# Performance work log

Hardware: AMD Instinct MI355X
Metric: run time of the kernel (lower is better)

## Reference

```python
import jax, jax.numpy as jnp
import numpy as np

L, H, C = 2, 8, 128          # layers, heads, hidden_channels
D = C // H                   # head dim
NPAT, NICD, NNDC = 50000, 591, 2042
OUT = 90
E = 250000                   # edges per relation
# edge relations as (src_type, dst_type); node types: 0=patient, 1=icd, 2=ndc
ETYPES = [(0, 1), (1, 0), (0, 2), (2, 0)]


def _seg_softmax(logits, seg, n):
    # softmax over edges grouped by destination node (PyG `softmax`)
    m = jax.ops.segment_max(logits, seg, num_segments=n)
    e = jnp.exp(logits - m[seg])
    s = jax.ops.segment_sum(e, seg, num_segments=n)
    return e / s[seg]


def setup_inputs() -> dict:
    key = jax.random.key(0)
    ks = jax.random.split(key, 24)
    s = 1.0 / np.sqrt(C)
    n = lambda k, shape, sc: jax.random.normal(k, shape, dtype=jnp.float32) * sc
    return {
        "x_patient": n(ks[0], (NPAT, C), 1.0),
        "w_in_patient": n(ks[1], (C, C), s),
        "b_in_patient": jnp.zeros((C,), jnp.float32),
        "emb_icd": n(ks[2], (NICD, C), 0.1),
        "emb_ndc": n(ks[3], (NNDC, C), 0.1),
        "kw": n(ks[4], (L, 3, C, C), s), "kb": jnp.zeros((L, 3, C), jnp.float32),
        "qw": n(ks[5], (L, 3, C, C), s), "qb": jnp.zeros((L, 3, C), jnp.float32),
        "vw": n(ks[6], (L, 3, C, C), s), "vb": jnp.zeros((L, 3, C), jnp.float32),
        "aw": n(ks[7], (L, 3, C, C), s), "ab": jnp.zeros((L, 3, C), jnp.float32),
        "skip": jnp.ones((L, 3), jnp.float32),
        "a_rel": n(ks[8], (L, 4, H, D, D), 1.0 / np.sqrt(D)),
        "m_rel": n(ks[9], (L, 4, H, D, D), 1.0 / np.sqrt(D)),
        "p_rel": jnp.ones((L, 4, H), jnp.float32),
        "w_out": n(ks[10], (C, OUT), s),
        "b_out": jnp.zeros((OUT,), jnp.float32),
        "x_icd": jnp.arange(NICD, dtype=jnp.int32),
        "x_ndc": jnp.arange(NNDC, dtype=jnp.int32),
        "src_pi": jax.random.randint(ks[11], (E,), 0, NPAT, dtype=jnp.int32),
        "dst_pi": jax.random.randint(ks[12], (E,), 0, NICD, dtype=jnp.int32),
        "src_ip": jax.random.randint(ks[13], (E,), 0, NICD, dtype=jnp.int32),
        "dst_ip": jax.random.randint(ks[14], (E,), 0, NPAT, dtype=jnp.int32),
        "src_pn": jax.random.randint(ks[15], (E,), 0, NPAT, dtype=jnp.int32),
        "dst_pn": jax.random.randint(ks[16], (E,), 0, NNDC, dtype=jnp.int32),
        "src_np": jax.random.randint(ks[17], (E,), 0, NNDC, dtype=jnp.int32),
        "dst_np": jax.random.randint(ks[18], (E,), 0, NPAT, dtype=jnp.int32),
    }


def reference(x_patient, w_in_patient, b_in_patient, emb_icd, emb_ndc,
              kw, kb, qw, qb, vw, vb, aw, ab, skip,
              a_rel, m_rel, p_rel, w_out, b_out,
              x_icd, x_ndc,
              src_pi, dst_pi, src_ip, dst_ip, src_pn, dst_pn, src_np, dst_np):
    edges = [(src_pi, dst_pi), (src_ip, dst_ip), (src_pn, dst_pn), (src_np, dst_np)]
    sizes = [NPAT, NICD, NNDC]
    # per-type input projection / embedding + relu
    x = [jax.nn.relu(x_patient @ w_in_patient + b_in_patient),
         jax.nn.relu(emb_icd[x_icd]),
         jax.nn.relu(emb_ndc[x_ndc])]
    scale = 1.0 / np.sqrt(D)
    for l in range(L):
        k = [(x[t] @ kw[l, t] + kb[l, t]).reshape(-1, H, D) for t in range(3)]
        q = [(x[t] @ qw[l, t] + qb[l, t]).reshape(-1, H, D) for t in range(3)]
        v = [(x[t] @ vw[l, t] + vb[l, t]).reshape(-1, H, D) for t in range(3)]
        agg = [jnp.zeros((sizes[t], H, D), x[0].dtype) for t in range(3)]
        for r, (st, dt) in enumerate(ETYPES):
            src, dst = edges[r]
            kr = jnp.einsum('nhd,hde->nhe', k[st], a_rel[l, r])  # relation key transform
            vr = jnp.einsum('nhd,hde->nhe', v[st], m_rel[l, r])  # relation msg transform
            alpha = jnp.sum(q[dt][dst] * kr[src], axis=-1) * p_rel[l, r] * scale  # [E,H]
            alpha = _seg_softmax(alpha, dst, sizes[dt])
            agg[dt] = agg[dt] + jax.ops.segment_sum(vr[src] * alpha[:, :, None], dst, num_segments=sizes[dt])
        new_x = []
        for t in range(3):
            o = jax.nn.gelu(agg[t].reshape(-1, C)) @ aw[l, t] + ab[l, t]
            a = jax.nn.sigmoid(skip[l, t])
            new_x.append(a * o + (1.0 - a) * x[t])  # learned skip (dims match)
        x = new_x
    return jax.nn.sigmoid(x[0] @ w_out + b_out)
```

## Files before the change

kernel.cpp:

```cpp
#include <hip/hip_runtime.h>
#include <math.h>

#define CDIM  128
#define NHEAD 8
#define DHEAD 16
#define NPAT  50000
#define NICD  591
#define NNDC  2042
#define OUTN  90
#define NEDGE 250000
#define NLAYER 2
#define ALC   640

#define OFF0  0
#define OFF1  (NICD)
#define OFF2  (NICD + NPAT)
#define OFF3  (NICD + NPAT + NNDC)
#define NTOT  (NICD + NPAT + NNDC + NPAT)
#define NB_SCAN ((NTOT + 1023) / 1024)

#define LDP 40
#define CTILE 72
#define LOG2E 1.4426950408889634f

#define NSEG  (2 * NNDC)
#define NAGG  ((NPAT + 3) / 4)

#define PB_W  224
#define PB_C  (PB_W + 16)
#define PB_Q  (PB_C + 3)
#define PB_Z  (PB_Q + NB_SCAN)
#define PB_G  (PB_Z + (((NICD + NNDC) * CDIM + 255) / 256))

#define SCAT_PER 64
#define SCAT_N   (4 * SCAT_PER)
#define INP_NWG  (((NPAT + 63) / 64) * 2)

typedef __attribute__((ext_vector_type(8))) short bf16x8;
typedef __attribute__((ext_vector_type(4))) float f32x4;

__device__ __forceinline__ float gelu_fast(float x) {
    float x3 = x * x * x;
    float y = 0.7978845608028654f * (x + 0.044715f * x3);
    float e = exp2f(y * (2.0f * LOG2E));
    float t = 1.0f - 2.0f * __builtin_amdgcn_rcpf(e + 1.0f);
    return 0.5f * x * (1.0f + t);
}
__device__ __forceinline__ float b2f(unsigned short u) {
    union { unsigned int i; float f; } v; v.i = ((unsigned int)u) << 16; return v.f;
}
__device__ __forceinline__ unsigned short f2b(float f) {
    union { float ff; unsigned int i; } v; v.ff = f;
    unsigned int i = v.i;
    return (unsigned short)((i + 0x7FFFu + ((i >> 16) & 1u)) >> 16);
}
__device__ __forceinline__ float2 b2x2(unsigned int u) {
    union { unsigned int i; float f; } lo, hi;
    lo.i = u << 16; hi.i = u & 0xFFFF0000u;
    return make_float2(lo.f, hi.f);
}

__device__ __forceinline__ void gemm_core(
    const unsigned short* __restrict__ Ap,
    const unsigned short* __restrict__ Wt, const float* __restrict__ bias,
    unsigned short* __restrict__ Cp, int ldc,
    int M, int N, int ntile, int wgid,
    const unsigned short* __restrict__ xold,
    const float* __restrict__ skipv, int skipidx,
    unsigned short* Al, unsigned short* Bl, unsigned short* Cst)
{
    int bm = (wgid / ntile) * 64, bn = (wgid % ntile) * 64;
    int t = threadIdx.x;
    int lane = t & 63, w = t >> 6;
    int wr = w >> 1, wc = w & 1;
    int quad = lane >> 4, lm = lane & 15;
    f32x4 acc[2][2] = {};
    const int srow = t >> 2;
    const int skq  = (t & 3) * 8;

    for (int k0 = 0; k0 < 128; k0 += 32) {
        {
            int row = bm + srow;
            uint4 u = make_uint4(0, 0, 0, 0);
            if (row < M)
                u = *(const uint4*)(Ap + (size_t)row * 128 + k0 + skq);
            *(uint4*)&Al[srow * LDP + skq] = u;
        }
        {
            int n = bn + srow;
            uint4 u = make_uint4(0, 0, 0, 0);
            if (n < N) u = *(const uint4*)(Wt + (size_t)n * 128 + k0 + skq);
            *(uint4*)&Bl[srow * LDP + skq] = u;
        }
        __syncthreads();
        bf16x8 af[2], bfr[2];
        #pragma unroll
        for (int i = 0; i < 2; i++) {
            af[i]  = *(const bf16x8*)&Al[(wr * 32 + i * 16 + lm) * LDP + quad * 8];
            bfr[i] = *(const bf16x8*)&Bl[(wc * 32 + i * 16 + lm) * LDP + quad * 8];
        }
        acc[0][0] = __builtin_amdgcn_mfma_f32_16x16x32_bf16(af[0], bfr[0], acc[0][0], 0, 0, 0);
        acc[0][1] = __builtin_amdgcn_mfma_f32_16x16x32_bf16(af[0], bfr[1], acc[0][1], 0, 0, 0);
        acc[1][0] = __builtin_amdgcn_mfma_f32_16x16x32_bf16(af[1], bfr[0], acc[1][0], 0, 0, 0);
        acc[1][1] = __builtin_amdgcn_mfma_f32_16x16x32_bf16(af[1], bfr[1], acc[1][1], 0, 0, 0);
        __syncthreads();
    }

    float aSk = 0.f, oneM = 0.f;
    if (skipv) {
        float sv = skipv[skipidx];
        aSk = 1.0f / (1.0f + expf(-sv));
        oneM = 1.0f - aSk;
    }
    #pragma unroll
    for (int tm = 0; tm < 2; tm++)
    #pragma unroll
    for (int tn = 0; tn < 2; tn++)
    #pragma unroll
    for (int r = 0; r < 4; r++) {
        int lrow = wr * 32 + tm * 16 + quad * 4 + r;
        int lcol = wc * 32 + tn * 16 + lm;
        int row = bm + lrow, col = bn + lcol;
        float v = acc[tm][tn][r] + (bias ? bias[col] : 0.f);
        if (skipv && row < M) v = aSk * v + oneM * b2f(xold[(size_t)row * ldc + col]);
        Cst[lrow * CTILE + lcol] = f2b(v);
    }
    __syncthreads();
    int row = t >> 2, seg = (t & 3) * 16;
    if (bm + row < M) {
        unsigned short* dst = Cp + (size_t)(bm + row) * ldc + bn + seg;
        *(uint4*)dst       = *(const uint4*)&Cst[row * CTILE + seg];
        *(uint4*)(dst + 8) = *(const uint4*)&Cst[row * CTILE + seg + 8];
    }
}

__device__ __forceinline__ void gemm3_body(
    int g,
    const unsigned short* A0, const unsigned short* W0,
    const float* b0, unsigned short* C0, int M0, int N0, int ntile0, int nwg0,
    const unsigned short* A1, const unsigned short* W1,
    const float* b1, unsigned short* C1, int M1, int N1, int ntile1, int nwg01,
    const unsigned short* A2, const unsigned short* W2,
    const float* b2, unsigned short* C2, int M2, int N2, int ntile2,
    const float* skipv, int si0, int si1, int si2,
    unsigned short* Al, unsigned short* Bl, unsigned short* Cst)
{
    if (g < nwg0) {
        int qq = nwg0 >> 3, rr = nwg0 & 7;
        int xcd = g & 7, idx = g >> 3;
        int wgid = (xcd < rr ? xcd * (qq + 1) : rr * (qq + 1) + (xcd - rr) * qq) + idx;
        gemm_core(A0, W0, b0, C0, N0, M0, N0, ntile0, wgid, C0, skipv, si0, Al, Bl, Cst);
    } else if (g < nwg01) {
        gemm_core(A1, W1, b1, C1, N1, M1, N1, ntile1, g - nwg0, C1, skipv, si1, Al, Bl, Cst);
    } else {
        gemm_core(A2, W2, b2, C2, N2, M2, N2, ntile2, g - nwg01, C2, skipv, si2, Al, Bl, Cst);
    }
}

__global__ __launch_bounds__(256) void gemm3_kernel(
    const unsigned short* __restrict__ A0, const unsigned short* __restrict__ W0,
    const float* __restrict__ b0, unsigned short* __restrict__ C0,
    int M0, int N0, int ntile0, int nwg0,
    const unsigned short* __restrict__ A1, const unsigned short* __restrict__ W1,
    const float* __restrict__ b1, unsigned short* __restrict__ C1,
    int M1, int N1, int ntile1, int nwg01,
    const unsigned short* __restrict__ A2, const unsigned short* __restrict__ W2,
    const float* __restrict__ b2, unsigned short* __restrict__ C2,
    int M2, int N2, int ntile2,
    const float* __restrict__ skipv, int si0, int si1, int si2)
{
    __shared__ unsigned short Al[64 * LDP];
    __shared__ unsigned short Bl[64 * LDP];
    __shared__ unsigned short Cst[64 * CTILE];
    gemm3_body(blockIdx.x, A0, W0, b0, C0, M0, N0, ntile0, nwg0,
               A1, W1, b1, C1, M1, N1, ntile1, nwg01,
               A2, W2, b2, C2, M2, N2, ntile2,
               skipv, si0, si1, si2, Al, Bl, Cst);
}

__device__ __forceinline__ void input_proj_body(
    int u, char* smem,
    const float* __restrict__ Axp, const unsigned short* __restrict__ Wtin,
    const float* __restrict__ b_in, unsigned short* __restrict__ xb0)
{
    unsigned short* Al = (unsigned short*)smem;
    unsigned short* Bl = Al + 64 * LDP;
    unsigned short* Cst = Bl + 64 * LDP;
    int t = threadIdx.x;
    int nwg = INP_NWG;
    int qq = nwg >> 3, rr = nwg & 7;
    int xcd = u & 7, idx = u >> 3;
    int wgid = (xcd < rr ? xcd * (qq + 1) : rr * (qq + 1) + (xcd - rr) * qq) + idx;
    int bm = (wgid >> 1) * 64, bn = (wgid & 1) * 64;

    int lane = t & 63, w = t >> 6;
    int wr = w >> 1, wc = w & 1;
    int quad = lane >> 4, lm = lane & 15;
    f32x4 acc[2][2] = {};
    const int srow = t >> 2;
    const int skq  = (t & 3) * 8;

    for (int k0 = 0; k0 < 128; k0 += 32) {
        {
            int row = bm + srow;
            float f[8] = {0.f,0.f,0.f,0.f,0.f,0.f,0.f,0.f};
            if (row < NPAT) {
                const float4* ap = (const float4*)(Axp + (size_t)row * 128 + k0 + skq);
                float4 u0 = ap[0], u1 = ap[1];
                f[0]=u0.x; f[1]=u0.y; f[2]=u0.z; f[3]=u0.w;
                f[4]=u1.x; f[5]=u1.y; f[6]=u1.z; f[7]=u1.w;
            }
            unsigned short v[8];
            for (int i = 0; i < 8; i++) v[i] = f2b(f[i]);
            *(uint4*)&Al[srow * LDP + skq] = *(uint4*)v;
        }
        {
            int n = bn + srow;
            *(uint4*)&Bl[srow * LDP + skq] = *(const uint4*)(Wtin + (size_t)n * 128 + k0 + skq);
        }
        __syncthreads();
        bf16x8 af[2], bfr[2];
        #pragma unroll
        for (int i = 0; i < 2; i++) {
            af[i]  = *(const bf16x8*)&Al[(wr * 32 + i * 16 + lm) * LDP + quad * 8];
            bfr[i] = *(const bf16x8*)&Bl[(wc * 32 + i * 16 + lm) * LDP + quad * 8];
        }
        acc[0][0] = __builtin_amdgcn_mfma_f32_16x16x32_bf16(af[0], bfr[0], acc[0][0], 0, 0, 0);
        acc[0][1] = __builtin_amdgcn_mfma_f32_16x16x32_bf16(af[0], bfr[1], acc[0][1], 0, 0, 0);
        acc[1][0] = __builtin_amdgcn_mfma_f32_16x16x32_bf16(af[1], bfr[0], acc[1][0], 0, 0, 0);
        acc[1][1] = __builtin_amdgcn_mfma_f32_16x16x32_bf16(af[1], bfr[1], acc[1][1], 0, 0, 0);
        __syncthreads();
    }
    #pragma unroll
    for (int tm = 0; tm < 2; tm++)
    #pragma unroll
    for (int tn = 0; tn < 2; tn++)
    #pragma unroll
    for (int r = 0; r < 4; r++) {
        int lrow = wr * 32 + tm * 16 + quad * 4 + r;
        int lcol = wc * 32 + tn * 16 + lm;
        float v = acc[tm][tn][r] + b_in[bn + lcol];
        v = fmaxf(v, 0.f);
        Cst[lrow * CTILE + lcol] = f2b(v);
    }
    __syncthreads();
    int row = t >> 2, seg = (t & 3) * 16;
    if (bm + row < NPAT) {
        unsigned short* dst = xb0 + (size_t)(bm + row) * 128 + bn + seg;
        *(uint4*)dst       = *(const uint4*)&Cst[row * CTILE + seg];
        *(uint4*)(dst + 8) = *(const uint4*)&Cst[row * CTILE + seg + 8];
    }
}

__device__ __forceinline__ void scatter_body(
    int b, char* smem,
    const int* s0, const int* d0, const int* s1, const int* d1,
    const int* s2, const int* d2, const int* s3, const int* d3,
    int* cursor, unsigned int* es)
{
    int t = threadIdx.x;
    int* lcnt = (int*)smem;
    int* lbase = lcnt + 2048;
    int rel = b / SCAT_PER;
    int bx = b % SCAT_PER;
    const int* sp = (rel == 0) ? s0 : (rel == 1) ? s1 : (rel == 2) ? s2 : s3;
    const int* dp = (rel == 0) ? d0 : (rel == 1) ? d1 : (rel == 2) ? d2 : d3;
    int off = (rel == 0) ? OFF0 : (rel == 1) ? OFF1 : (rel == 2) ? OFF2 : OFF3;
    if (rel == 1 || rel == 3) {
        for (int e = bx * 256 + t; e < NEDGE; e += SCAT_PER * 256) {
            int d = dp[e];
            int p = atomicAdd(&cursor[off + d], 1);
            es[p] = ((unsigned int)sp[e] << 16) | (unsigned int)d;
        }
    } else {
        int nb = (rel == 0) ? NICD : NNDC;
        int per = (NEDGE + SCAT_PER - 1) / SCAT_PER;
        int e0 = bx * per, e1 = min(e0 + per, NEDGE);
        for (int i = t; i < nb; i += 256) lcnt[i] = 0;
        __syncthreads();
        for (int e = e0 + t; e < e1; e += 256) atomicAdd(&lcnt[dp[e]], 1);
        __syncthreads();
        for (int i = t; i < nb; i += 256) {
            int c = lcnt[i];
            lbase[i] = c ? atomicAdd(&cursor[off + i], c) : 0;
            lcnt[i] = 0;
        }
        __syncthreads();
        for (int e = e0 + t; e < e1; e += 256) {
            int d = dp[e];
            int p = lbase[d] + atomicAdd(&lcnt[d], 1);
            es[p] = ((unsigned int)sp[e] << 16) | (unsigned int)d;
        }
    }
}

__global__ __launch_bounds__(256) void hist_in_kernel(
    const int* __restrict__ d0, const int* __restrict__ d1,
    const int* __restrict__ d2, const int* __restrict__ d3,
    int* __restrict__ deg,
    const float* __restrict__ Axp, const unsigned short* __restrict__ Wtin,
    const float* __restrict__ b_in, unsigned short* __restrict__ xb0)
{
    __shared__ __align__(16) char smem[19456];
    int b = blockIdx.x;
    int t = threadIdx.x;
    if (b < 256) {
        int* lh = (int*)smem;
        int rel = b >> 6;
        int bx = b & 63;
        const int* dp = (rel == 0) ? d0 : (rel == 1) ? d1 : (rel == 2) ? d2 : d3;
        int off = (rel == 0) ? OFF0 : (rel == 1) ? OFF1 : (rel == 2) ? OFF2 : OFF3;
        if (rel == 1 || rel == 3) {
            for (int e = bx * 256 + t; e < NEDGE; e += 64 * 256)
                atomicAdd(&deg[off + dp[e]], 1);
        } else {
            int nb = (rel == 0) ? NICD : NNDC;
            for (int i = t; i < nb; i += 256) lh[i] = 0;
            __syncthreads();
            for (int e = bx * 256 + t; e < NEDGE; e += 64 * 256)
                atomicAdd(&lh[dp[e]], 1);
            __syncthreads();
            for (int i = t; i < nb; i += 256) {
                int v = lh[i];
                if (v) atomicAdd(&deg[off + i], v);
            }
        }
    } else {
        input_proj_body(b - 256, smem, Axp, Wtin, b_in, xb0);
// ... 47 lines not shown
    int qq = nwg >> 3, rr = nwg & 7;
    int xcd = orig & 7, idx = orig >> 3;
    int wgid = (xcd < rr ? xcd * (qq + 1) : rr * (qq + 1) + (xcd - rr) * qq) + idx;
    int bm = (wgid / ntile) * 64, bn = (wgid % ntile) * 64;

    int t = threadIdx.x;
    int lane = t & 63, w = t >> 6;
    int wr = w >> 1, wc = w & 1;
    int quad = lane >> 4, lm = lane & 15;
    f32x4 acc[2][2] = {};
    const int srow = t >> 2;
    const int skq  = (t & 3) * 8;

    for (int k0 = 0; k0 < 128; k0 += 32) {
        {
            int row = bm + srow;
            uint4 u = make_uint4(0, 0, 0, 0);
            if (a_mode == 0) {
                if (row < M)
                    u = *(const uint4*)((const unsigned short*)Ap + (size_t)row * lda + k0 + skq);
            } else {
                float f[8] = {0.f,0.f,0.f,0.f,0.f,0.f,0.f,0.f};
                if (row < M) {
                    const float4* ap = (const float4*)((const float*)Ap + (size_t)row * lda + k0 + skq);
                    float4 u0 = ap[0], u1 = ap[1];
                    f[0]=u0.x; f[1]=u0.y; f[2]=u0.z; f[3]=u0.w;
                    f[4]=u1.x; f[5]=u1.y; f[6]=u1.z; f[7]=u1.w;
                }
                unsigned short v[8];
                for (int i = 0; i < 8; i++) v[i] = f2b(f[i]);
                u = *(uint4*)v;
            }
            *(uint4*)&Al[srow * LDP + skq] = u;
        }
        {
            int n = bn + srow;
            uint4 u = make_uint4(0, 0, 0, 0);
            if (n < N) u = *(const uint4*)(Wt + (size_t)n * 128 + k0 + skq);
            *(uint4*)&Bl[srow * LDP + skq] = u;
        }
        __syncthreads();
        bf16x8 af[2], bfr[2];
        #pragma unroll
        for (int i = 0; i < 2; i++) {
            af[i]  = *(const bf16x8*)&Al[(wr * 32 + i * 16 + lm) * LDP + quad * 8];
            bfr[i] = *(const bf16x8*)&Bl[(wc * 32 + i * 16 + lm) * LDP + quad * 8];
        }
        acc[0][0] = __builtin_amdgcn_mfma_f32_16x16x32_bf16(af[0], bfr[0], acc[0][0], 0, 0, 0);
        acc[0][1] = __builtin_amdgcn_mfma_f32_16x16x32_bf16(af[0], bfr[1], acc[0][1], 0, 0, 0);
        acc[1][0] = __builtin_amdgcn_mfma_f32_16x16x32_bf16(af[1], bfr[0], acc[1][0], 0, 0, 0);
        acc[1][1] = __builtin_amdgcn_mfma_f32_16x16x32_bf16(af[1], bfr[1], acc[1][1], 0, 0, 0);
        __syncthreads();
    }

    if (c_mode == 0) {
        #pragma unroll
        for (int tm = 0; tm < 2; tm++)
        #pragma unroll
        for (int tn = 0; tn < 2; tn++)
        #pragma unroll
        for (int r = 0; r < 4; r++) {
            int lrow = wr * 32 + tm * 16 + quad * 4 + r;
            int lcol = wc * 32 + tn * 16 + lm;
            int col = bn + lcol;
            float v = acc[tm][tn][r] + (bias ? bias[col] : 0.f);
            if (act == 1) v = fmaxf(v, 0.f);
            Cst[lrow * CTILE + lcol] = f2b(v);
        }
        __syncthreads();
        int row = t >> 2, seg = (t & 3) * 16;
        if (bm + row < M) {
            unsigned short* dst = (unsigned short*)Cp + (size_t)(bm + row) * ldc + bn + seg;
            *(uint4*)dst       = *(const uint4*)&Cst[row * CTILE + seg];
            *(uint4*)(dst + 8) = *(const uint4*)&Cst[row * CTILE + seg + 8];
        }
    } else {
        #pragma unroll
        for (int tm = 0; tm < 2; tm++)
        #pragma unroll
        for (int tn = 0; tn < 2; tn++)
        #pragma unroll
        for (int r = 0; r < 4; r++) {
            int row = bm + wr * 32 + tm * 16 + quad * 4 + r;
            int col = bn + wc * 32 + tn * 16 + lm;
            if (row >= M || col >= N) continue;
            float v = acc[tm][tn][r] + (bias ? bias[col] : 0.f);
            if (act == 1) v = fmaxf(v, 0.f);
            else if (act == 2) v = 1.0f / (1.0f + expf(-v));
            ((float*)Cp)[(size_t)row * ldc + col] = v;
        }
    }
}

__global__ __launch_bounds__(256) void prep_all_kernel(
    const float* __restrict__ qw, const float* __restrict__ aw,
    const float* __restrict__ w_in, const float* __restrict__ w_out,
    unsigned short* __restrict__ Wb0, unsigned short* __restrict__ Wb1,
    unsigned short* __restrict__ Wb2, unsigned short* __restrict__ Wtaw,
    unsigned short* __restrict__ Wtin, unsigned short* __restrict__ Wtout,
    const float* __restrict__ kw, const float* __restrict__ vw,
    const float* __restrict__ a_rel, const float* __restrict__ m_rel,
    const float* __restrict__ kb, const float* __restrict__ vb,
    float* __restrict__ bb0, float* __restrict__ bb1, float* __restrict__ bb2,
    const float* __restrict__ qb,
    int* __restrict__ deg,
    const float* __restrict__ emb_icd, const int* __restrict__ x_icd,
    unsigned short* __restrict__ xb1,
    const float* __restrict__ emb_ndc, const int* __restrict__ x_ndc,
    unsigned short* __restrict__ xb2)
{
    __shared__ float tile[32][33];
    int b = blockIdx.x;
    int tid = threadIdx.x;
    if (b < PB_W) {
        int z = b >> 4, rem = b & 15;
        int by = rem >> 2, bx = rem & 3;
        const float* s; unsigned short* d; int N = 128;
        if (z < 2)       { s = qw + (size_t)z * 3 * 16384;               d = Wb0 + (size_t)z * 640 * 128; }
        else if (z < 4)  { s = qw + 16384 + (size_t)(z - 2) * 3 * 16384; d = Wb1 + (size_t)(z - 2) * 384 * 128; }
        else if (z < 6)  { s = qw + 2 * 16384 + (size_t)(z - 4) * 3 * 16384; d = Wb2 + (size_t)(z - 4) * 384 * 128; }
        else if (z < 12) { s = aw + (size_t)(z - 6) * 16384;             d = Wtaw + (size_t)(z - 6) * 16384; }
        else if (z == 12){ s = w_in;  d = Wtin; }
        else             { s = w_out; d = Wtout; N = OUTN; }
        int k0 = bx * 32, n0 = by * 32;
        int tx = tid & 31, ty = tid >> 5;
        for (int i = 0; i < 32; i += 8) {
            int k = k0 + ty + i, n = n0 + tx;
            tile[ty + i][tx] = (k < 128 && n < N) ? s[(size_t)k * N + n] : 0.f;
        }
        __syncthreads();
        for (int i = 0; i < 32; i += 8) {
            int n = n0 + ty + i, k = k0 + tx;
            if (n < N && k < 128) d[(size_t)n * 128 + k] = f2b(tile[tx][ty + i]);
        }
    } else if (b < PB_C) {
        int s = b - PB_W;
        int l = s >> 3, j = s & 7;
        int ty, isV, r, rowoff, nw;
        unsigned short* Wb; float* bb;
        switch (j) {
          case 0: ty=0; isV=0; r=0; Wb=Wb0; bb=bb0; rowoff=128; nw=640; break;
          case 1: ty=0; isV=1; r=0; Wb=Wb0; bb=bb0; rowoff=256; nw=640; break;
          case 2: ty=0; isV=0; r=2; Wb=Wb0; bb=bb0; rowoff=384; nw=640; break;
          case 3: ty=0; isV=1; r=2; Wb=Wb0; bb=bb0; rowoff=512; nw=640; break;
          case 4: ty=1; isV=0; r=1; Wb=Wb1; bb=bb1; rowoff=128; nw=384; break;
          case 5: ty=1; isV=1; r=1; Wb=Wb1; bb=bb1; rowoff=256; nw=384; break;
          case 6: ty=2; isV=0; r=3; Wb=Wb2; bb=bb2; rowoff=128; nw=384; break;
          default:ty=2; isV=1; r=3; Wb=Wb2; bb=bb2; rowoff=256; nw=384; break;
        }
        const float* W = (isV ? vw : kw) + (size_t)(l * 3 + ty) * 16384;
        const float* A = (isV ? m_rel : a_rel) + (size_t)(l * 4 + r) * 2048;
        const float* B = (isV ? vb : kb) + (size_t)(l * 3 + ty) * 128;
        unsigned short* dst = Wb + (size_t)l * nw * 128 + (size_t)rowoff * 128;
        float* bdst = bb + (size_t)l * nw + rowoff;
        int n = tid & 127;
        int kh = tid >> 7;
        int h = n >> 4, e = n & 15;
        float Ar[16];
        #pragma unroll
        for (int d = 0; d < 16; d++) Ar[d] = A[h * 256 + d * 16 + e];
        for (int k = kh * 64; k < kh * 64 + 64; k++) {
            float acc = 0.f;
            const float* wr = W + (size_t)k * 128 + h * 16;
            #pragma unroll
            for (int d = 0; d < 16; d++) acc += wr[d] * Ar[d];
            dst[(size_t)n * 128 + k] = f2b(acc);
        }
        if (kh == 0) {
            float acc = 0.f;
            const float* br = B + h * 16;
            #pragma unroll
            for (int d = 0; d < 16; d++) acc += br[d] * Ar[d];
            bdst[n] = acc;
        }
    } else if (b < PB_Q) {
        int t = (b - PB_C) * 256 + tid;
        if (t < 6 * 128) {
            int g = t >> 7, c = t & 127;
            int l = g / 3, ty = g % 3;
            float v = qb[g * 128 + c];
            if (ty == 0) bb0[l * 640 + c] = v;
            else if (ty == 1) bb1[l * 384 + c] = v;
            else bb2[l * 384 + c] = v;
        }
    } else if (b < PB_Z) {
        int base = (b - PB_Q) * 1024 + tid * 4;
        if (base + 3 < NTOT) *(int4*)(deg + base) = make_int4(0, 0, 0, 0);
        else for (int i = 0; i < 4; i++) if (base + i < NTOT) deg[base + i] = 0;
    } else {
        int t = (b - PB_Z) * 256 + tid;
        int totA = NICD * CDIM;
        if (t < totA) {
            int r = t >> 7, c = t & 127;
            xb1[t] = f2b(fmaxf(emb_icd[(size_t)x_icd[r] * CDIM + c], 0.f));
        } else if (t < totA + NNDC * CDIM) {
            int u = t - totA;
            int r = u >> 7, c = u & 127;
            xb2[u] = f2b(fmaxf(emb_ndc[(size_t)x_ndc[r] * CDIM + c], 0.f));
        }
    }
}

__global__ __launch_bounds__(256) void scanA_kernel(
    const int* __restrict__ deg, int* __restrict__ part, int n)
{
    __shared__ int red[256];
    int b = blockIdx.x, t = threadIdx.x;
    int base = b * 1024 + t * 4;
    int s = 0;
    if (base + 3 < n) {
        int4 v = *(const int4*)(deg + base);
        s = v.x + v.y + v.z + v.w;
    } else {
        for (int i = 0; i < 4; i++) if (base + i < n) s += deg[base + i];
    }
    red[t] = s;
    __syncthreads();
    for (int o = 128; o; o >>= 1) { if (t < o) red[t] += red[t + o]; __syncthreads(); }
    if (t == 0) part[b] = red[0];
}

__global__ __launch_bounds__(256) void scanC2_kernel(
    const int* __restrict__ deg, const int* __restrict__ part,
    int* __restrict__ rp0, int* __restrict__ rp1,
    int* __restrict__ rp2, int* __restrict__ rp3,
    int* __restrict__ cursor, int n)
{
    __shared__ int red[256];
    __shared__ int pre[128];
    int b = blockIdx.x, t = threadIdx.x;
    if (t < 128) pre[t] = (t < b) ? part[t] : 0;
    __syncthreads();
    for (int o = 64; o; o >>= 1) { if (t < o) pre[t] += pre[t + o]; __syncthreads(); }
    int pbase = pre[0];
    __syncthreads();

    int base = b * 1024 + t * 4;
    int v[4] = {0, 0, 0, 0};
    if (base + 3 < n) {
        int4 q = *(const int4*)(deg + base);
        v[0] = q.x; v[1] = q.y; v[2] = q.z; v[3] = q.w;
    } else {
        for (int i = 0; i < 4; i++) if (base + i < n) v[i] = deg[base + i];
    }
    red[t] = v[0] + v[1] + v[2] + v[3];
    __syncthreads();
    for (int off = 1; off < 256; off <<= 1) {
        int y = (t >= off) ? red[t - off] : 0;
        __syncthreads();
        red[t] += y;
        __syncthreads();
    }
    int run = pbase + ((t == 0) ? 0 : red[t - 1]);
    for (int i = 0; i < 4; i++) {
        int g = base + i;
        if (g < n) {
            cursor[g] = run;
            int r, loc;
            if      (g < OFF1) { r = 0; loc = g; }
            else if (g < OFF2) { r = 1; loc = g - OFF1; }
            else if (g < OFF3) { r = 2; loc = g - OFF2; }
            else               { r = 3; loc = g - OFF3; }
            int Sl = run - r * NEDGE;
            ((r == 0) ? rp0 : (r == 1) ? rp1 : (r == 2) ? rp2 : rp3)[loc] = Sl;
            run += v[i];
        }
    }
    if (b == 0 && t == 0) {
        rp0[NICD] = NEDGE; rp1[NPAT] = NEDGE; rp2[NNDC] = NEDGE; rp3[NPAT] = NEDGE;
    }
}

__device__ __forceinline__ float dot16_bf(const unsigned short* a,
                                          const unsigned short* b) {
    const uint4* ap = (const uint4*)a;
    const uint4* bp = (const uint4*)b;
    uint4 a0 = ap[0], a1 = ap[1], b0 = bp[0], b1 = bp[1];
    unsigned int au[8] = {a0.x, a0.y, a0.z, a0.w, a1.x, a1.y, a1.z, a1.w};
    unsigned int bu[8] = {b0.x, b0.y, b0.z, b0.w, b1.x, b1.y, b1.z, b1.w};
    float acc = 0.f;
    #pragma unroll
    for (int j = 0; j < 8; j++) {
        float2 x = b2x2(au[j]), y = b2x2(bu[j]);
        acc += x.x * y.x + x.y * y.y;
    }
    return acc;
}

__device__ __forceinline__ float dot16_q(uint4 a0, uint4 a1,
                                         const unsigned short* b) {
    const uint4* bp = (const uint4*)b;
    uint4 b0 = bp[0], b1 = bp[1];
    unsigned int au[8] = {a0.x, a0.y, a0.z, a0.w, a1.x, a1.y, a1.z, a1.w};
    unsigned int bu[8] = {b0.x, b0.y, b0.z, b0.w, b1.x, b1.y, b1.z, b1.w};
    float acc = 0.f;
    #pragma unroll
    for (int j = 0; j < 8; j++) {
        float2 x = b2x2(au[j]), y = b2x2(bu[j]);
        acc += x.x * y.x + x.y * y.y;
    }
    return acc;
}

__global__ __launch_bounds__(256) void seg_kernel(
    const int* __restrict__ rpA, const unsigned int* __restrict__ esA,
    const unsigned short* __restrict__ qA, int ldqA,
    const unsigned short* __restrict__ krA, const unsigned short* __restrict__ vrA, int ldsA,
    const float* __restrict__ prelA, float* __restrict__ alphaA,
    unsigned short* __restrict__ aggA, int ndA,
    const int* __restrict__ rpB, const unsigned int* __restrict__ esB,
    const unsigned short* __restrict__ qB, int ldqB,
    const unsigned short* __restrict__ krB, const unsigned short* __restrict__ vrB, int ldsB,
    const float* __restrict__ prelB, float* __restrict__ alphaB,
    unsigned short* __restrict__ aggB, int ndB)
{
    __shared__ float wred[4][8];
    __shared__ float sinv[8];
    __shared__ float p3f[4][64][2];
    __shared__ float wl[ALC * NHEAD];
    __shared__ unsigned short sl[ALC];
    int rel = blockIdx.y;
    int n = blockIdx.x;
    const int* rp            = rel ? rpB : rpA;
    const unsigned int* es   = rel ? esB : esA;
    const unsigned short* q  = rel ? qB : qA;
    int ldq                  = rel ? ldqB : ldqA;
    const unsigned short* kr = rel ? krB : krA;
    const unsigned short* vr = rel ? vrB : vrA;
    int ldsrc                = rel ? ldsB : ldsA;
    const float* prel        = rel ? prelB : prelA;
    float* alpha             = rel ? alphaB : alphaA;
    unsigned short* agg      = rel ? aggB : aggA;
    int nd                   = rel ? ndB : ndA;
    if (n >= nd) return;

    int r0 = rp[n], deg = rp[n + 1] - r0;
    int t = threadIdx.x;
    int h = t & 7, j = t >> 3;
    int lane = t & 63, wv = t >> 6;
    const unsigned short* qrow = q + (size_t)n * ldq + h * DHEAD;
    uint4 qa = ((const uint4*)qrow)[0], qb = ((const uint4*)qrow)[1];
    float ph = prel[h] * 0.25f * LOG2E;

    if (deg <= ALC) {
        for (int i = t; i < deg; i += 256) sl[i] = (unsigned short)(es[r0 + i] >> 16);
        __syncthreads();

        float mx = -1e30f;
        int i = j;
        for (; i + 96 < deg; i += 128) {
            int s0 = sl[i], s1 = sl[i + 32], s2 = sl[i + 64], s3 = sl[i + 96];
            float a0 = dot16_q(qa, qb, kr + (size_t)s0 * ldsrc + h * DHEAD) * ph;
            float a1 = dot16_q(qa, qb, kr + (size_t)s1 * ldsrc + h * DHEAD) * ph;
            float a2 = dot16_q(qa, qb, kr + (size_t)s2 * ldsrc + h * DHEAD) * ph;
            float a3 = dot16_q(qa, qb, kr + (size_t)s3 * ldsrc + h * DHEAD) * ph;
            wl[(i)      * NHEAD + h] = a0;
            wl[(i + 32) * NHEAD + h] = a1;
            wl[(i + 64) * NHEAD + h] = a2;
            wl[(i + 96) * NHEAD + h] = a3;
            mx = fmaxf(mx, fmaxf(fmaxf(a0, a1), fmaxf(a2, a3)));
        }
        for (; i < deg; i += 32) {
            int s0 = sl[i];
            float a = dot16_q(qa, qb, kr + (size_t)s0 * ldsrc + h * DHEAD) * ph;
            wl[i * NHEAD + h] = a;
            mx = fmaxf(mx, a);
        }
        mx = fmaxf(mx, __shfl_xor(mx, 8));
        mx = fmaxf(mx, __shfl_xor(mx, 16));
        mx = fmaxf(mx, __shfl_xor(mx, 32));
        if (lane < 8) wred[wv][h] = mx;
        __syncthreads();
        float m = fmaxf(fmaxf(wred[0][h], wred[1][h]), fmaxf(wred[2][h], wred[3][h]));
        __syncthreads();

        float sm = 0.f;
        for (i = j; i < deg; i += 32) {
            float e = exp2f(wl[i * NHEAD + h] - m);
            wl[i * NHEAD + h] = e;
            sm += e;
        }
        sm += __shfl_xor(sm, 8);
        sm += __shfl_xor(sm, 16);
        sm += __shfl_xor(sm, 32);
        if (lane < 8) wred[wv][h] = sm;
        __syncthreads();
        if (t < 8) {
            float s = wred[0][t] + wred[1][t] + wred[2][t] + wred[3][t];
            sinv[t] = (s > 0.f) ? 1.0f / s : 0.f;
        }
        __syncthreads();

        int g = t >> 6, l = t & 63;
        int hh = l >> 3;
        float acc0 = 0.f, acc1 = 0.f;
        i = g;
        for (; i + 28 < deg; i += 32) {
            int e0 = sl[i],      e1 = sl[i + 4],  e2 = sl[i + 8],  e3 = sl[i + 12];
            int e4 = sl[i + 16], e5 = sl[i + 20], e6 = sl[i + 24], e7 = sl[i + 28];
            unsigned int u0 = *(const unsigned int*)(vr + (size_t)e0 * ldsrc + 2 * l);
            unsigned int u1 = *(const unsigned int*)(vr + (size_t)e1 * ldsrc + 2 * l);
            unsigned int u2 = *(const unsigned int*)(vr + (size_t)e2 * ldsrc + 2 * l);
            unsigned int u3 = *(const unsigned int*)(vr + (size_t)e3 * ldsrc + 2 * l);
            unsigned int u4 = *(const unsigned int*)(vr + (size_t)e4 * ldsrc + 2 * l);
            unsigned int u5 = *(const unsigned int*)(vr + (size_t)e5 * ldsrc + 2 * l);
            unsigned int u6 = *(const unsigned int*)(vr + (size_t)e6 * ldsrc + 2 * l);
            unsigned int u7 = *(const unsigned int*)(vr + (size_t)e7 * ldsrc + 2 * l);
            float w0 = wl[(i)      * NHEAD + hh], w1 = wl[(i + 4)  * NHEAD + hh];
            float w2 = wl[(i + 8)  * NHEAD + hh], w3 = wl[(i + 12) * NHEAD + hh];
            float w4 = wl[(i + 16) * NHEAD + hh], w5 = wl[(i + 20) * NHEAD + hh];
            float w6 = wl[(i + 24) * NHEAD + hh], w7 = wl[(i + 28) * NHEAD + hh];
            float2 v0 = b2x2(u0), v1 = b2x2(u1), v2 = b2x2(u2), v3 = b2x2(u3);
            float2 v4 = b2x2(u4), v5 = b2x2(u5), v6 = b2x2(u6), v7 = b2x2(u7);
            acc0 += w0 * v0.x + w1 * v1.x + w2 * v2.x + w3 * v3.x
                  + w4 * v4.x + w5 * v5.x + w6 * v6.x + w7 * v7.x;
            acc1 += w0 * v0.y + w1 * v1.y + w2 * v2.y + w3 * v3.y
                  + w4 * v4.y + w5 * v5.y + w6 * v6.y + w7 * v7.y;
        }
        for (; i < deg; i += 4) {
            int e0 = sl[i];
            unsigned int u0 = *(const unsigned int*)(vr + (size_t)e0 * ldsrc + 2 * l);
            float w0 = wl[i * NHEAD + hh];
            float2 v0 = b2x2(u0);
            acc0 += w0 * v0.x;
            acc1 += w0 * v0.y;
        }
        p3f[g][l][0] = acc0;
        p3f[g][l][1] = acc1;
        __syncthreads();
        if (t < 128) {
            int c = t;
            float v = p3f[0][c >> 1][c & 1] + p3f[1][c >> 1][c & 1]
                    + p3f[2][c >> 1][c & 1] + p3f[3][c >> 1][c & 1];
            agg[(size_t)n * CDIM + c] = f2b(gelu_fast(v * sinv[c >> 4]));
        }
    } else {
        float* p3 = (float*)p3f;
        float mx = -1e30f;
        for (int i = j; i < deg; i += 32) {
            int sn = es[r0 + i] >> 16;
            float a = dot16_q(qa, qb, kr + (size_t)sn * ldsrc + h * DHEAD) * ph;
            alpha[(size_t)(r0 + i) * NHEAD + h] = a;
            mx = fmaxf(mx, a);
        }
        mx = fmaxf(mx, __shfl_xor(mx, 8));
        mx = fmaxf(mx, __shfl_xor(mx, 16));
        mx = fmaxf(mx, __shfl_xor(mx, 32));
        if (lane < 8) wred[wv][h] = mx;
        __syncthreads();
        float m = fmaxf(fmaxf(wred[0][h], wred[1][h]), fmaxf(wred[2][h], wred[3][h]));
        __syncthreads();

        float sm = 0.f;
        for (int i = j; i < deg; i += 32) {
            size_t ai = (size_t)(r0 + i) * NHEAD + h;
            float e = exp2f(alpha[ai] - m);
            alpha[ai] = e;
            sm += e;
        }
        sm += __shfl_xor(sm, 8);
        sm += __shfl_xor(sm, 16);
        sm += __shfl_xor(sm, 32);
        if (lane < 8) wred[wv][h] = sm;
        __syncthreads();
        if (t < 8) {
            float s = wred[0][t] + wred[1][t] + wred[2][t] + wred[3][t];
            sinv[t] = (s > 0.f) ? 1.0f / s : 0.f;
        }
        __syncthreads();

        int c = t & 127, half = t >> 7;
        float hsi = sinv[c >> 4];
        float acc = 0.f;
        int i = half;
        for (; i + 6 < deg; i += 8) {
            unsigned int e0 = es[r0 + i],     e1 = es[r0 + i + 2];
            unsigned int e2 = es[r0 + i + 4], e3 = es[r0 + i + 6];
            float w0 = alpha[(size_t)(r0 + i)     * NHEAD + (c >> 4)];
            float w1 = alpha[(size_t)(r0 + i + 2) * NHEAD + (c >> 4)];
            float w2 = alpha[(size_t)(r0 + i + 4) * NHEAD + (c >> 4)];
            float w3 = alpha[(size_t)(r0 + i + 6) * NHEAD + (c >> 4)];
            float v0 = b2f(vr[(size_t)(e0 >> 16) * ldsrc + c]);
            float v1 = b2f(vr[(size_t)(e1 >> 16) * ldsrc + c]);
            float v2 = b2f(vr[(size_t)(e2 >> 16) * ldsrc + c]);
            float v3 = b2f(vr[(size_t)(e3 >> 16) * ldsrc + c]);
            acc += w0 * v0 + w1 * v1 + w2 * v2 + w3 * v3;
        }
        for (; i < deg; i += 2) {
            unsigned int e0 = es[r0 + i];
            float w0 = alpha[(size_t)(r0 + i) * NHEAD + (c >> 4)];
            acc += w0 * b2f(vr[(size_t)(e0 >> 16) * ldsrc + c]);
        }
        p3[t] = acc * hsi;
        __syncthreads();
        if (half == 0) agg[(size_t)n * CDIM + c] = f2b(gelu_fast(p3[c] + p3[128 + c]));
    }
}

__global__ __launch_bounds__(256) void agg2_kernel(
    const int* __restrict__ rp1, const unsigned int* __restrict__ es1,
    const int* __restrict__ rp3, const unsigned int* __restrict__ es3,
    const unsigned short* __restrict__ q, int ldq,
    const unsigned short* __restrict__ kr1, const unsigned short* __restrict__ vr1, int ld1,
    const unsigned short* __restrict__ kr3, const unsigned short* __restrict__ vr3, int ld3,
    const float* __restrict__ prel1, const float* __restrict__ prel3,
    unsigned short* __restrict__ agg, int nd)
{
    __shared__ float wls[4][128 * NHEAD];
    __shared__ int slo[4][128];
    int wv  = threadIdx.x >> 6;
    int wid = (blockIdx.x * 256 + threadIdx.x) >> 6;
    int lane = threadIdx.x & 63;
    if (wid >= nd) return;
    float* wl = wls[wv];
    int* sl = slo[wv];
    int h = lane & 7, j = lane >> 3;
    int hc = lane >> 3;
    const unsigned short* qbase = q + (size_t)wid * ldq;

    int r0a = rp1[wid], degA = rp1[wid + 1] - r0a;
    int r0b = rp3[wid], degB = rp3[wid + 1] - r0b;

    float o0, o1;
    if (degA <= 64 && degB <= 64) {
        const unsigned short* qrow = qbase + h * DHEAD;
        uint4 qa = ((const uint4*)qrow)[0], qb = ((const uint4*)qrow)[1];
        float phA = prel1[h] * 0.25f * LOG2E;
        float phB = prel3[h] * 0.25f * LOG2E;
        int dOfs = (int)(kr3 - kr1);
        float mA = -1e30f, mB = -1e30f;
        for (int i = j; i < degA; i += 8) {
            int sn = es1[r0a + i] >> 16;
            int off = sn * ld1;
            float a = dot16_q(qa, qb, kr1 + off + h * DHEAD) * phA;
            wl[i * NHEAD + h] = a;
            if (h == 0) sl[i] = off;
            mA = fmaxf(mA, a);
        }
        for (int i = j; i < degB; i += 8) {
            int sn = es3[r0b + i] >> 16;
            int off = sn * ld3;
            float a = dot16_q(qa, qb, kr3 + off + h * DHEAD) * phB;
            wl[(degA + i) * NHEAD + h] = a;
            if (h == 0) sl[degA + i] = dOfs + off;
            mB = fmaxf(mB, a);
        }
        mA = fmaxf(mA, __shfl_xor(mA, 8));   mB = fmaxf(mB, __shfl_xor(mB, 8));
        mA = fmaxf(mA, __shfl_xor(mA, 16));  mB = fmaxf(mB, __shfl_xor(mB, 16));
        mA = fmaxf(mA, __shfl_xor(mA, 32));  mB = fmaxf(mB, __shfl_xor(mB, 32));

        int dtot = degA + degB;
        float sA = 0.f, sB = 0.f;
        for (int i = j; i < dtot; i += 8) {
            bool isA = i < degA;
            float e = exp2f(wl[i * NHEAD + h] - (isA ? mA : mB));
            wl[i * NHEAD + h] = e;
            sA += isA ? e : 0.f;
            sB += isA ? 0.f : e;
        }
        sA += __shfl_xor(sA, 8);   sB += __shfl_xor(sB, 8);
        sA += __shfl_xor(sA, 16);  sB += __shfl_xor(sB, 16);
        sA += __shfl_xor(sA, 32);  sB += __shfl_xor(sB, 32);
        float siA = (sA > 0.f) ? 1.0f / sA : 0.f;
        float siB = (sB > 0.f) ? 1.0f / sB : 0.f;
        float siAh = __shfl(siA, hc);
        float siBh = __shfl(siB, hc);

        float accA0 = 0.f, accA1 = 0.f, accB0 = 0.f, accB1 = 0.f;
        int i = 0;
        for (; i + 4 <= degA; i += 4) {
            int oo0 = sl[i + 0], oo1 = sl[i + 1], oo2 = sl[i + 2], oo3 = sl[i + 3];
            unsigned int u0 = *(const unsigned int*)(vr1 + oo0 + 2 * lane);
            unsigned int u1 = *(const unsigned int*)(vr1 + oo1 + 2 * lane);
            unsigned int u2 = *(const unsigned int*)(vr1 + oo2 + 2 * lane);
            unsigned int u3 = *(const unsigned int*)(vr1 + oo3 + 2 * lane);
            float w0 = wl[(i + 0) * NHEAD + hc];
            float w1 = wl[(i + 1) * NHEAD + hc];
            float w2 = wl[(i + 2) * NHEAD + hc];
            float w3 = wl[(i + 3) * NHEAD + hc];
            float2 v0 = b2x2(u0), v1 = b2x2(u1), v2 = b2x2(u2), v3 = b2x2(u3);
            accA0 += w0 * v0.x + w1 * v1.x + w2 * v2.x + w3 * v3.x;
            accA1 += w0 * v0.y + w1 * v1.y + w2 * v2.y + w3 * v3.y;
        }
        for (; i < degA; i++) {
            int oo = sl[i];
            unsigned int u0 = *(const unsigned int*)(vr1 + oo + 2 * lane);
            float w0 = wl[i * NHEAD + hc];
            float2 v0 = b2x2(u0);
            accA0 += w0 * v0.x; accA1 += w0 * v0.y;
        }
        for (; i + 4 <= dtot; i += 4) {
            int oo0 = sl[i + 0], oo1 = sl[i + 1], oo2 = sl[i + 2], oo3 = sl[i + 3];
            unsigned int u0 = *(const unsigned int*)(vr1 + oo0 + 2 * lane);
            unsigned int u1 = *(const unsigned int*)(vr1 + oo1 + 2 * lane);
            unsigned int u2 = *(const unsigned int*)(vr1 + oo2 + 2 * lane);
            unsigned int u3 = *(const unsigned int*)(vr1 + oo3 + 2 * lane);
            float w0 = wl[(i + 0) * NHEAD + hc];
            float w1 = wl[(i + 1) * NHEAD + hc];
            float w2 = wl[(i + 2) * NHEAD + hc];
            float w3 = wl[(i + 3) * NHEAD + hc];
            float2 v0 = b2x2(u0), v1 = b2x2(u1), v2 = b2x2(u2), v3 = b2x2(u3);
            accB0 += w0 * v0.x + w1 * v1.x + w2 * v2.x + w3 * v3.x;
            accB1 += w0 * v0.y + w1 * v1.y + w2 * v2.y + w3 * v3.y;
        }
        for (; i < dtot; i++) {
            int oo = sl[i];
            unsigned int u0 = *(const unsigned int*)(vr1 + oo + 2 * lane);
            float w0 = wl[i * NHEAD + hc];
            float2 v0 = b2x2(u0);
            accB0 += w0 * v0.x; accB1 += w0 * v0.y;
        }
        o0 = accA0 * siAh + accB0 * siBh;
        o1 = accA1 * siAh + accB1 * siBh;
    } else {
        float acc0 = 0.f, acc1 = 0.f;
        #pragma unroll
        for (int rr = 0; rr < 2; rr++) {
            const unsigned int* es = rr ? es3 : es1;
            const unsigned short* kr = rr ? kr3 : kr1;
            const unsigned short* vr = rr ? vr3 : vr1;
            int ld = rr ? ld3 : ld1;
            const float* prel = rr ? prel3 : prel1;
            int r0 = rr ? r0b : r0a;
            int deg = rr ? degB : degA;
            if (deg <= 0) continue;
            const unsigned short* qrow = qbase + h * DHEAD;
            float ph = prel[h] * 0.25f * LOG2E;
            bool small = (deg <= 64);

            float m = -1e30f;
            for (int i = j; i < deg; i += 8) {
                int sn = es[r0 + i] >> 16;
                float a = dot16_bf(qrow, kr + (size_t)sn * ld + h * DHEAD) * ph;
                if (small) wl[i * NHEAD + h] = a;
                m = fmaxf(m, a);
            }
            m = fmaxf(m, __shfl_xor(m, 8));
            m = fmaxf(m, __shfl_xor(m, 16));
            m = fmaxf(m, __shfl_xor(m, 32));
            float s = 0.f;
            for (int i = j; i < deg; i += 8) {
                float a;
                if (small) a = wl[i * NHEAD + h];
                else {
                    int sn = es[r0 + i] >> 16;
                    a = dot16_bf(qrow, kr + (size_t)sn * ld + h * DHEAD) * ph;
                }
                float e = exp2f(a - m);
                if (small) wl[i * NHEAD + h] = e;
                s += e;
            }
            s += __shfl_xor(s, 8);
            s += __shfl_xor(s, 16);
            s += __shfl_xor(s, 32);
            float si = (s > 0.f) ? 1.0f / s : 0.f;
            if (small)
                for (int i = j; i < deg; i += 8)
                    wl[i * NHEAD + h] *= si;

            float m_hc  = __shfl(m, hc);
            float si_hc = __shfl(si, hc);
            float ph_hc = __shfl(ph, hc);
            const unsigned short* qrow_hc = qbase + hc * DHEAD;
            for (int i = 0; i < deg; i++) {
                unsigned int sv = es[r0 + i] >> 16;
                unsigned int pv = *(const unsigned int*)(vr + (size_t)sv * ld + 2 * lane);
                float2 v = b2x2(pv);
                float wgt;
                if (small) wgt = wl[i * NHEAD + hc];
                else {
                    float a = dot16_bf(qrow_hc, kr + (size_t)sv * ld + hc * DHEAD) * ph_hc;
                    wgt = exp2f(a - m_hc) * si_hc;
                }
                acc0 += wgt * v.x;
                acc1 += wgt * v.y;
            }
        }
        o0 = acc0; o1 = acc1;
    }
    unsigned int packed = (unsigned int)f2b(gelu_fast(o0))
                        | ((unsigned int)f2b(gelu_fast(o1)) << 16);
    *(unsigned int*)(agg + (size_t)wid * CDIM + 2 * lane) = packed;
}

extern "C" void kernel_launch(void* const* d_in, const int* in_sizes, int n_in,
                              void* d_out, int out_size, void* d_ws, size_t ws_size,
                              hipStream_t stream)
{
    const float* x_patient = (const float*)d_in[0];
    const float* w_in      = (const float*)d_in[1];
    const float* b_in      = (const float*)d_in[2];
    const float* emb_icd   = (const float*)d_in[3];
    const float* emb_ndc   = (const float*)d_in[4];
    const float* kw        = (const float*)d_in[5];
    const float* kbias     = (const float*)d_in[6];
    const float* qw        = (const float*)d_in[7];
    const float* qbias     = (const float*)d_in[8];
    const float* vw        = (const float*)d_in[9];
    const float* vbias     = (const float*)d_in[10];
    const float* aw        = (const float*)d_in[11];
    const float* abias     = (const float*)d_in[12];
    const float* skip      = (const float*)d_in[13];
    const float* a_rel     = (const float*)d_in[14];
    const float* m_rel     = (const float*)d_in[15];
    const float* p_rel     = (const float*)d_in[16];
    const float* w_out     = (const float*)d_in[17];
    const float* b_out     = (const float*)d_in[18];
    const int*   x_icd     = (const int*)d_in[19];
    const int*   x_ndc     = (const int*)d_in[20];
    const int* esrc[4] = {(const int*)d_in[21], (const int*)d_in[23],
                          (const int*)d_in[25], (const int*)d_in[27]};
    const int* edst[4] = {(const int*)d_in[22], (const int*)d_in[24],
                          (const int*)d_in[26], (const int*)d_in[28]};

    const int sizes[3] = {NPAT, NICD, NNDC};

    char* p = (char*)d_ws;
    auto alloc = [&](size_t bytes) -> void* {
        void* r = (void*)p;
        p += (bytes + 255) & ~(size_t)255;
        return r;
    };

    unsigned short *xb[3];
    for (int t = 0; t < 3; t++) xb[t] = (unsigned short*)alloc((size_t)sizes[t] * CDIM * 2);
    unsigned short* P0 = (unsigned short*)alloc((size_t)NPAT * 640 * 2);
    unsigned short* P1 = (unsigned short*)alloc((size_t)NICD * 384 * 2);
    unsigned short* P2 = (unsigned short*)alloc((size_t)NNDC * 384 * 2);
    unsigned short* aggbase = (unsigned short*)alloc((size_t)(NPAT + NICD + NNDC) * CDIM * 2);
    unsigned short* agg[3];
    agg[0] = aggbase;
    agg[1] = aggbase + (size_t)NPAT * CDIM;
    agg[2] = agg[1] + (size_t)NICD * CDIM;
    float*  alphabuf  = (float*)alloc((size_t)NEDGE * NHEAD * 4);
    float*  alphabuf2 = (float*)alloc((size_t)NEDGE * NHEAD * 4);
    unsigned int* esbig = (unsigned int*)alloc((size_t)4 * NEDGE * 4);
    int* rowptr[4];
    rowptr[0] = (int*)alloc((size_t)(NICD + 1) * 4);
    rowptr[1] = (int*)alloc((size_t)(NPAT + 1) * 4);
    rowptr[2] = (int*)alloc((size_t)(NNDC + 1) * 4);
    rowptr[3] = (int*)alloc((size_t)(NPAT + 1) * 4);
    int* deg    = (int*)alloc((size_t)NTOT * 4);
    int* cursor = (int*)alloc((size_t)NTOT * 4);
    int* part   = (int*)alloc((size_t)256 * 4);
    unsigned short* Wb0   = (unsigned short*)alloc((size_t)2 * 640 * 128 * 2);
    unsigned short* Wb1   = (unsigned short*)alloc((size_t)2 * 384 * 128 * 2);
    unsigned short* Wb2   = (unsigned short*)alloc((size_t)2 * 384 * 128 * 2);
    unsigned short* Wtaw  = (unsigned short*)alloc((size_t)6 * 128 * 128 * 2);
    unsigned short* Wtin  = (unsigned short*)alloc((size_t)128 * 128 * 2);
    unsigned short* Wtout = (unsigned short*)alloc((size_t)OUTN * 128 * 2);
    float* bb0 = (float*)alloc((size_t)2 * 640 * 4);
    float* bb1 = (float*)alloc((size_t)2 * 384 * 4);
    float* bb2 = (float*)alloc((size_t)2 * 384 * 4);
    unsigned int* esRel[4];
    for (int r = 0; r < 4; r++) esRel[r] = esbig + (size_t)r * NEDGE;

    const int ntP0 = 640 / 64, nwgP0 = ((NPAT + 63) / 64) * ntP0;
    const int ntP1 = 384 / 64, nwgP1 = ((NICD + 63) / 64) * ntP1;
    const int ntP2 = 384 / 64, nwgP2 = ((NNDC + 63) / 64) * ntP2;
    const int ntS  = 128 / 64;
    const int nwgS0 = ((NPAT + 63) / 64) * ntS;
    const int nwgS1 = ((NICD + 63) / 64) * ntS;
    const int nwgS2 = ((NNDC + 63) / 64) * ntS;

    prep_all_kernel<<<dim3(PB_G), dim3(256), 0, stream>>>(
        qw, aw, w_in, w_out, Wb0, Wb1, Wb2, Wtaw, Wtin, Wtout,
        kw, vw, a_rel, m_rel, kbias, vbias, bb0, bb1, bb2, qbias,
        deg, emb_icd, x_icd, xb[1], emb_ndc, x_ndc, xb[2]);

    hist_in_kernel<<<dim3(256 + INP_NWG), dim3(256), 0, stream>>>(
        edst[0], edst[1], edst[2], edst[3], deg,
        x_patient, Wtin, b_in, xb[0]);

    scanA_kernel<<<NB_SCAN, 256, 0, stream>>>(deg, part, NTOT);
    scanC2_kernel<<<NB_SCAN, 256, 0, stream>>>(deg, part,
        rowptr[0], rowptr[1], rowptr[2], rowptr[3], cursor, NTOT);

    scat_proj_kernel<<<dim3(SCAT_N + nwgP0 + nwgP1 + nwgP2), dim3(256), 0, stream>>>(
        esrc[0], edst[0], esrc[1], edst[1], esrc[2], edst[2], esrc[3], edst[3],
        cursor, esbig,
        xb[0], Wb0, bb0, P0, NPAT, 640, ntP0, nwgP0,
        xb[1], Wb1, bb1, P1, NICD, 384, ntP1, nwgP0 + nwgP1,
        xb[2], Wb2, bb2, P2, NNDC, 384, ntP2);

    for (int l = 0; l < NLAYER; l++) {
        if (l > 0) {
            gemm3_kernel<<<dim3(nwgP0 + nwgP1 + nwgP2), dim3(256), 0, stream>>>(
                xb[0], Wb0 + (size_t)l * 640 * 128, bb0 + (size_t)l * 640, P0,
                NPAT, 640, ntP0, nwgP0,
                xb[1], Wb1 + (size_t)l * 384 * 128, bb1 + (size_t)l * 384, P1,
                NICD, 384, ntP1, nwgP0 + nwgP1,
                xb[2], Wb2 + (size_t)l * 384 * 128, bb2 + (size_t)l * 384, P2,
                NNDC, 384, ntP2,
                nullptr, 0, 0, 0);
        }

        seg_kernel<<<dim3(NNDC, 2), dim3(256), 0, stream>>>(
            rowptr[0], esRel[0], P1, 384, P0 + 128, P0 + 256, 640,
            p_rel + (size_t)(l * 4 + 0) * NHEAD, alphabuf, agg[1], NICD,
            rowptr[2], esRel[2], P2, 384, P0 + 384, P0 + 512, 640,
            p_rel + (size_t)(l * 4 + 2) * NHEAD, alphabuf2, agg[2], NNDC);

        agg2_kernel<<<dim3(NAGG), dim3(256), 0, stream>>>(
            rowptr[1], esRel[1], rowptr[3], esRel[3],
            P0, 640, P1 + 128, P1 + 256, 384, P2 + 128, P2 + 256, 384,
            p_rel + (size_t)(l * 4 + 1) * NHEAD, p_rel + (size_t)(l * 4 + 3) * NHEAD,
            agg[0], NPAT);

        gemm3_kernel<<<dim3(nwgS0 + nwgS1 + nwgS2), dim3(256), 0, stream>>>(
            agg[0], Wtaw + (size_t)(l * 3 + 0) * 16384, abias + (size_t)(l * 3 + 0) * 128, xb[0],
            NPAT, 128, ntS, nwgS0,
            agg[1], Wtaw + (size_t)(l * 3 + 1) * 16384, abias + (size_t)(l * 3 + 1) * 128, xb[1],
            NICD, 128, ntS, nwgS0 + nwgS1,
            agg[2], Wtaw + (size_t)(l * 3 + 2) * 16384, abias + (size_t)(l * 3 + 2) * 128, xb[2],
            NNDC, 128, ntS,
            skip, l * 3 + 0, l * 3 + 1, l * 3 + 2);
    }

    {
        int ntile = (OUTN + 63) / 64;
        int nwg = ((NPAT + 63) / 64) * ntile;
        gemm_xs<<<dim3(nwg), dim3(256), 0, stream>>>(xb[0], 0, 128, Wtout, b_out,
            d_out, 1, OUTN, NPAT, OUTN, 2, ntile, nullptr, 0, nullptr, 0);
    }
}
```

Baseline: 467.8 us.

## Fuse seg and agg2 edge kernels into one launch with shared smem

Merges the destination-segment kernel (icd/ndc) and the patient aggregation kernel into a single launch whose blocks branch on blockIdx, using one shared-memory buffer carved up per role. The seg grid also drops from NNDC×2 blocks, which left many icd blocks idle, to exactly NICD+NNDC blocks. ALC shrinks from 640 to 512 so the union smem stays small, which raises the number of blocks that can be resident at once. This removes a launch and the idle tail between the two kernels, so the long seg blocks can overlap with the many small agg blocks. The cost is that the smaller ALC may push more high-degree nodes onto the fallback path.

Measured after the change: 495.7 us. 1.06x slower.

```diff
diff --git a/kernel.cpp b/kernel.cpp
--- a/kernel.cpp
+++ b/kernel.cpp
@@ -10,7 +10,7 @@
 #define OUTN  90
 #define NEDGE 250000
 #define NLAYER 2
-#define ALC   640
+#define ALC   512
 
 #define OFF0  0
 #define OFF1  (NICD)
@@ -23,7 +23,7 @@
 #define CTILE 72
 #define LOG2E 1.4426950408889634f
 
-#define NSEG  (2 * NNDC)
+#define NED2  (NICD + NNDC)
 #define NAGG  ((NPAT + 3) / 4)
 
 #define PB_W  224
@@ -677,7 +677,8 @@
     return acc;
 }
 
-__global__ __launch_bounds__(256) void seg_kernel(
+__device__ void seg_body(
+    int rel, int n, char* smem,
     const int* __restrict__ rpA, const unsigned int* __restrict__ esA,
     const unsigned short* __restrict__ qA, int ldqA,
     const unsigned short* __restrict__ krA, const unsigned short* __restrict__ vrA, int ldsA,
@@ -689,13 +690,12 @@
     const float* __restrict__ prelB, float* __restrict__ alphaB,
     unsigned short* __restrict__ aggB, int ndB)
 {
-    __shared__ float wred[4][8];
-    __shared__ float sinv[8];
-    __shared__ float p3f[4][64][2];
-    __shared__ float wl[ALC * NHEAD];
-    __shared__ unsigned short sl[ALC];
-    int rel = blockIdx.y;
-    int n = blockIdx.x;
+    float (*wred)[8] = (float(*)[8])smem;
+    float* sinv = (float*)(smem + 128);
+    float (*p3f)[64][2] = (float(*)[64][2])(smem + 160);
+    float* wl = (float*)(smem + 2208);
+    unsigned short* sl = (unsigned short*)(smem + 18592);
+
     const int* rp            = rel ? rpB : rpA;
     const unsigned int* es   = rel ? esB : esA;
     const unsigned short* q  = rel ? qB : qA;
@@ -872,7 +872,8 @@
     }
 }
 
-__global__ __launch_bounds__(256) void agg2_kernel(
+__device__ void agg2_body(
+    int lb, char* smem,
     const int* __restrict__ rp1, const unsigned int* __restrict__ es1,
     const int* __restrict__ rp3, const unsigned int* __restrict__ es3,
     const unsigned short* __restrict__ q, int ldq,
@@ -881,14 +882,14 @@
     const float* __restrict__ prel1, const float* __restrict__ prel3,
     unsigned short* __restrict__ agg, int nd)
 {
-    __shared__ float wls[4][128 * NHEAD];
-    __shared__ int slo[4][128];
+    float* wls = (float*)smem;
+    int* slo = (int*)(smem + 16384);
     int wv  = threadIdx.x >> 6;
-    int wid = (blockIdx.x * 256 + threadIdx.x) >> 6;
+    int wid = lb * 4 + wv;
     int lane = threadIdx.x & 63;
     if (wid >= nd) return;
-    float* wl = wls[wv];
-    int* sl = slo[wv];
+    float* wl = wls + wv * 128 * NHEAD;
+    int* sl = slo + wv * 128;
     int h = lane & 7, j = lane >> 3;
     int hc = lane >> 3;
     const unsigned short* qbase = q + (size_t)wid * ldq;
@@ -1056,6 +1057,42 @@
     unsigned int packed = (unsigned int)f2b(gelu_fast(o0))
                         | ((unsigned int)f2b(gelu_fast(o1)) << 16);
     *(unsigned int*)(agg + (size_t)wid * CDIM + 2 * lane) = packed;
+}
+
+__global__ __launch_bounds__(256) void edge2_kernel(
+    const int* __restrict__ rpA, const unsigned int* __restrict__ esA,
+    const unsigned short* __restrict__ qA, int ldqA,
+    const unsigned short* __restrict__ krA, const unsigned short* __restrict__ vrA, int ldsA,
+    const float* __restrict__ prelA, float* __restrict__ alphaA,
+    unsigned short* __restrict__ aggA, int ndA,
+    const int* __restrict__ rpB, const unsigned int* __restrict__ esB,
+    const unsigned short* __restrict__ qB, int ldqB,
+    const unsigned short* __restrict__ krB, const unsigned short* __restrict__ vrB, int ldsB,
+    const float* __restrict__ prelB, float* __restrict__ alphaB,
+    unsigned short* __restrict__ aggB, int ndB,
+    const int* __restrict__ rp1, const unsigned int* __restrict__ es1,
+    const int* __restrict__ rp3, const unsigned int* __restrict__ es3,
+    const unsigned short* __restrict__ qP, int ldqP,
+    const unsigned short* __restrict__ kr1, const unsigned short* __restrict__ vr1, int ld1,
+    const unsigned short* __restrict__ kr3, const unsigned short* __restrict__ vr3, int ld3,
+    const float* __restrict__ prel1, const float* __restrict__ prel3,
+    unsigned short* __restrict__ aggP, int ndP)
+{
+    __shared__ __align__(16) char smem[19616];
+    int b = blockIdx.x;
+    if (b < NICD) {
+        seg_body(0, b, smem,
+                 rpA, esA, qA, ldqA, krA, vrA, ldsA, prelA, alphaA, aggA, ndA,
+                 rpB, esB, qB, ldqB, krB, vrB, ldsB, prelB, alphaB, aggB, ndB);
+    } else if (b < NED2) {
+        seg_body(1, b - NICD, smem,
+                 rpA, esA, qA, ldqA, krA, vrA, ldsA, prelA, alphaA, aggA, ndA,
+                 rpB, esB, qB, ldqB, krB, vrB, ldsB, prelB, alphaB, aggB, ndB);
+    } else {
+        agg2_body(b - NED2, smem,
+                  rp1, es1, rp3, es3, qP, ldqP, kr1, vr1, ld1, kr3, vr3, ld3,
+                  prel1, prel3, aggP, ndP);
+    }
 }
 
 extern "C" void kernel_launch(void* const* d_in, const int* in_sizes, int n_in,
@@ -1170,13 +1207,11 @@
                 nullptr, 0, 0, 0);
         }
 
-        seg_kernel<<<dim3(NNDC, 2), dim3(256), 0, stream>>>(
+        edge2_kernel<<<dim3(NED2 + NAGG), dim3(256), 0, stream>>>(
             rowptr[0], esRel[0], P1, 384, P0 + 128, P0 + 256, 640,
             p_rel + (size_t)(l * 4 + 0) * NHEAD, alphabuf, agg[1], NICD,
             rowptr[2], esRel[2], P2, 384, P0 + 384, P0 + 512, 640,
-            p_rel + (size_t)(l * 4 + 2) * NHEAD, alphabuf2, agg[2], NNDC);
-
-        agg2_kernel<<<dim3(NAGG), dim3(256), 0, stream>>>(
+            p_rel + (size_t)(l * 4 + 2) * NHEAD, alphabuf2, agg[2], NNDC,
             rowptr[1], esRel[1], rowptr[3], esRel[3],
             P0, 640, P1 + 128, P1 + 256, 384, P2 + 128, P2 + 256, 384,
             p_rel + (size_t)(l * 4 + 1) * NHEAD, p_rel + (size_t)(l * 4 + 3) * NHEAD,
```
